# Optimization experiments

Measured on AMD Instinct MI355X. Metric: run time of the kernel, lower is better.

## Reference

```python
import jax, jax.numpy as jnp
import numpy as np

TEMPERATURE = 0.07
NEG_INF = -9e15
EPS = 1e-12

def setup_inputs() -> dict:
    key = jax.random.key(0)
    k1, k2 = jax.random.split(key)
    N, D = 8192, 128
    features = jax.random.normal(k1, (N, D), dtype=jnp.float32)
    labels = jax.random.randint(k2, (N,), 0, 16, dtype=jnp.int64)
    return {"features": features, "labels": labels}

def reference(features, labels):
    N = features.shape[0]
    # L2 normalize rows (torch F.normalize: x / max(||x||, eps))
    norm = jnp.linalg.norm(features, axis=1, keepdims=True)
    f = features / jnp.maximum(norm, EPS)
    # [N, N] similarity
    sim = jnp.matmul(f, f.T) / TEMPERATURE
    eye = jnp.eye(N, dtype=bool)
    sim = jnp.where(eye, NEG_INF, sim)
    # positive-pair mask: same label, excluding self
    pos_mask = ((labels[:, None] == labels[None, :]) & ~eye).astype(sim.dtype)
    denom = jnp.exp(sim).sum(axis=1, keepdims=True)  # [N, 1]
    log_prob = sim - jnp.log(denom + EPS)
    loss = -(pos_mask * log_prob).sum(axis=1) / (pos_mask.sum(axis=1) + EPS)
    return loss.mean()
```

## Files before the change

### kernel.cpp

```cpp
#include <hip/hip_runtime.h>
#include <hip/hip_bf16.h>

#define EPS 1e-12f
#define SQRT_C_EXP 4.53981597f
#define M_LN2F 0.69314718056f

#define BM 256
#define BN 128
#define KD 128
#define NCHUNK 8
#define NPART 16
#define PSTRIDE 48

typedef __attribute__((ext_vector_type(4))) float f32x4;
typedef __attribute__((ext_vector_type(8))) short bf16x8;

__device__ __forceinline__ float bf2f(ushort u) {
    unsigned int x = ((unsigned int)u) << 16;
    return __uint_as_float(x);
}

__device__ __forceinline__ void gload16(const void* g, void* l) {
    __builtin_amdgcn_global_load_lds(
        (const __attribute__((address_space(1))) void*)g,
        (__attribute__((address_space(3))) void*)l, 16, 0, 0);
}

__device__ __forceinline__ const bf16x8* lds_frag(const ushort* base, int r, int slot) {
    int sw = slot ^ (r & 7);
    return reinterpret_cast<const bf16x8*>(
        reinterpret_cast<const char*>(base) + r * 256 + sw * 16);
}

__global__ void normalize_kernel(const float* __restrict__ feat,
                                 ushort* __restrict__ fb,
                                 float* __restrict__ sq,
                                 int N) {
    int r    = (blockIdx.x * blockDim.x + threadIdx.x) >> 6;
    int lane = threadIdx.x & 63;
    if (r >= N) return;
    const float2 v = *reinterpret_cast<const float2*>(feat + (size_t)r * KD + lane * 2);
    float s = v.x * v.x + v.y * v.y;
    #pragma unroll
    for (int off = 1; off < 64; off <<= 1) s += __shfl_xor(s, off);
    const float scale = SQRT_C_EXP / fmaxf(sqrtf(s), EPS);

    __hip_bfloat16 h0 = __float2bfloat16(v.x * scale);
    __hip_bfloat16 h1 = __float2bfloat16(v.y * scale);
    ushort u0 = *reinterpret_cast<ushort*>(&h0);
    ushort u1 = *reinterpret_cast<ushort*>(&h1);
    unsigned int pack = (unsigned int)u0 | ((unsigned int)u1 << 16);
    *reinterpret_cast<unsigned int*>(fb + (size_t)r * KD + lane * 2) = pack;

    float q0 = bf2f(u0), q1 = bf2f(u1);
    float q = q0 * q0 + q1 * q1;
    #pragma unroll
    for (int off = 1; off < 64; off <<= 1) q += __shfl_xor(q, off);
    if (lane == 0) sq[r] = q;
}

__global__ __launch_bounds__(512)
__attribute__((amdgpu_waves_per_eu(2, 2)))
void supcon_denom(
    const ushort* __restrict__ fb,
    const int* __restrict__ labels,
    float* __restrict__ part,
    int N) {

    __shared__ __align__(16) ushort As[BM * KD];
    __shared__ __align__(16) ushort Bs[2][BN * KD];

    const int tid  = threadIdx.x;
    const int lane = tid & 63;
    const int w    = tid >> 6;
    const int wr   = w >> 1;
    const int wc   = w & 1;
    const int r16  = lane & 15;
    const int g4   = lane >> 4;

    const int rowbase = blockIdx.y * BM;
    const int col0    = blockIdx.x * (BN * NCHUNK);

    {
        const ushort* gA = fb + (size_t)rowbase * KD;
        #pragma unroll
        for (int i = 0; i < 8; i++) {
            int d = i * 512 + tid;
            int s = d ^ ((d >> 4) & 7);
            gload16(gA + (size_t)s * 8, &As[d * 8]);
        }
        const ushort* gB = fb + (size_t)col0 * KD;
        #pragma unroll
        for (int i = 0; i < 4; i++) {
            int d = i * 512 + tid;
            int s = d ^ ((d >> 4) & 7);
            gload16(gB + (size_t)s * 8, &Bs[0][d * 8]);
        }
    }

    int rlab[4][4];
    #pragma unroll
    for (int m = 0; m < 4; m++)
        #pragma unroll
        for (int i = 0; i < 4; i++)
            rlab[m][i] = labels[rowbase + wr * 64 + m * 16 + g4 * 4 + i];

    __syncthreads();

    bf16x8 a[4][4];
    #pragma unroll
    for (int ks = 0; ks < 4; ks++) {
        const int slot = ks * 4 + g4;
        #pragma unroll
        for (int m = 0; m < 4; m++)
            a[ks][m] = *lds_frag(As, wr * 64 + m * 16 + r16, slot);
    }

    float pd[4][4], pp[4][4], pc[4][4];
    #pragma unroll
    for (int m = 0; m < 4; m++)
        #pragma unroll
        for (int i = 0; i < 4; i++) { pd[m][i] = 0.f; pp[m][i] = 0.f; pc[m][i] = 0.f; }

    int cur = 0;
    for (int c = 0; c < NCHUNK; c++) {
        if (c + 1 < NCHUNK) {
            const ushort* gB = fb + (size_t)(col0 + (c + 1) * BN) * KD;
            ushort* dstb = Bs[cur ^ 1];
            #pragma unroll
            for (int i = 0; i < 4; i++) {
                int d = i * 512 + tid;
                int s = d ^ ((d >> 4) & 7);
                gload16(gB + (size_t)s * 8, &dstb[d * 8]);
            }
        }

        const ushort* bbase = Bs[cur];
        const int colbase = col0 + c * BN + wc * 64;

        #pragma unroll 1
        for (int n = 0; n < 4; n++) {
            const int clab = labels[colbase + n * 16 + r16];

            f32x4 acc[4];
            #pragma unroll
            for (int m = 0; m < 4; m++) acc[m] = f32x4{0.f, 0.f, 0.f, 0.f};

            #pragma unroll
            for (int ks = 0; ks < 4; ks++) {
                const int slot = ks * 4 + g4;
                bf16x8 bv = *lds_frag(bbase, wc * 64 + n * 16 + r16, slot);
                #pragma unroll
                for (int m = 0; m < 4; m++)
                    acc[m] = __builtin_amdgcn_mfma_f32_16x16x32_bf16(a[ks][m], bv, acc[m], 0, 0, 0);
            }

            #pragma unroll
            for (int m = 0; m < 4; m++)
                #pragma unroll
                for (int i = 0; i < 4; i++) {
                    const float sim = acc[m][i];
                    pd[m][i] += __builtin_amdgcn_exp2f(sim);
                    const bool mt = (rlab[m][i] == clab);
                    pp[m][i] += mt ? sim : 0.f;
                    pc[m][i] += mt ? 1.f : 0.f;
                }
        }

        __syncthreads();
        cur ^= 1;
    }

    #pragma unroll
    for (int off = 1; off < 16; off <<= 1)
        #pragma unroll
        for (int m = 0; m < 4; m++)
            #pragma unroll
            for (int i = 0; i < 4; i++) {
                pd[m][i] += __shfl_xor(pd[m][i], off);
                pp[m][i] += __shfl_xor(pp[m][i], off);
                pc[m][i] += __shfl_xor(pc[m][i], off);
            }

    if (r16 == 0) {
        const int slot = blockIdx.x * 2 + wc;
        #pragma unroll
        for (int m = 0; m < 4; m++)
            #pragma unroll
            for (int i = 0; i < 4; i++) {
                int r = rowbase + wr * 64 + m * 16 + g4 * 4 + i;
                float* p = part + (size_t)r * PSTRIDE + slot;
                p[0]  = pd[m][i];
                p[16] = pp[m][i];
                p[32] = pc[m][i];
            }
    }
}

__global__ void rowloss_kernel(const float* __restrict__ part,
                               const float* __restrict__ sq,
                               float* __restrict__ rowloss,
                               int N) {
    int r    = (blockIdx.x * blockDim.x + threadIdx.x) >> 6;
    int lane = threadIdx.x & 63;
    if (r >= N) return;

    float v = (lane < PSTRIDE) ? part[(size_t)r * PSTRIDE + lane] : 0.f;
    #pragma unroll
    for (int off = 1; off < 16; off <<= 1) v += __shfl_xor(v, off);
    float dsum = __shfl(v, 0);
    float psum = __shfl(v, 16);
    float csum = __shfl(v, 32);

    if (lane == 0) {
        float sqr    = sq[r];
        float possum = (psum - sqr) * M_LN2F;
        float cnt    = csum - 1.0f;
        float dn     = dsum - __builtin_amdgcn_exp2f(sqr);
        rowloss[r]   = -(possum - cnt * logf(dn + EPS)) / (cnt + EPS);
    }
}

__global__ void reduce_kernel(const float* __restrict__ rowloss,
                              float* __restrict__ out, int N) {
    __shared__ float sdata[16];
    float s = 0.f;
    for (int r = threadIdx.x; r < N; r += blockDim.x) s += rowloss[r];
    #pragma unroll
    for (int off = 1; off < 64; off <<= 1) s += __shfl_xor(s, off);
    int wv = threadIdx.x >> 6;
    if ((threadIdx.x & 63) == 0) sdata[wv] = s;
    __syncthreads();
    if (threadIdx.x == 0) {
        float t = 0.f;
        int nw = (int)(blockDim.x >> 6);
        for (int i = 0; i < nw; i++) t += sdata[i];
        out[0] = t / (float)N;
    }
}

extern "C" void kernel_launch(void* const* d_in, const int* in_sizes, int n_in,
                              void* d_out, int out_size, void* d_ws, size_t ws_size,
                              hipStream_t stream) {
    const float* feat = (const float*)d_in[0];
    const int* labels = (const int*)d_in[1];
    const int N = in_sizes[1];

    char* ws = (char*)d_ws;
    size_t off = 0;
    ushort* fb     = (ushort*)(ws + off);  off += (size_t)N * KD * sizeof(ushort);
    float* sq      = (float*)(ws + off);   off += (size_t)N * sizeof(float);
    float* part    = (float*)(ws + off);   off += (size_t)N * PSTRIDE * sizeof(float);
    float* rowloss = (float*)(ws + off);

    normalize_kernel<<<(N + 3) / 4, 256, 0, stream>>>(feat, fb, sq, N);

    dim3 grid(N / (BN * NCHUNK), N / BM);
    supcon_denom<<<grid, 512, 0, stream>>>(fb, labels, part, N);

    rowloss_kernel<<<(N + 3) / 4, 256, 0, stream>>>(part, sq, rowloss, N);
    reduce_kernel<<<1, 1024, 0, stream>>>(rowloss, (float*)d_out, N);
}
```

Baseline: 48.43 us.

## Compute positive counts from a class histogram and process two column tiles per iteration

```diff
diff --git a/kernel.cpp b/kernel.cpp
--- a/kernel.cpp
+++ b/kernel.cpp
@@ -4,13 +4,13 @@
 #define EPS 1e-12f
 #define SQRT_C_EXP 4.53981597f
 #define M_LN2F 0.69314718056f
+#define NUM_CLASSES 16
 
 #define BM 256
 #define BN 128
 #define KD 128
 #define NCHUNK 8
-#define NPART 16
-#define PSTRIDE 48
+#define PSTRIDE 32
 
 typedef __attribute__((ext_vector_type(4))) float f32x4;
 typedef __attribute__((ext_vector_type(8))) short bf16x8;
@@ -33,30 +33,61 @@
 }
 
 __global__ void normalize_kernel(const float* __restrict__ feat,
+                                 const int* __restrict__ labels,
                                  ushort* __restrict__ fb,
                                  float* __restrict__ sq,
+                                 float* __restrict__ cnt16,
                                  int N) {
-    int r    = (blockIdx.x * blockDim.x + threadIdx.x) >> 6;
-    int lane = threadIdx.x & 63;
-    if (r >= N) return;
-    const float2 v = *reinterpret_cast<const float2*>(feat + (size_t)r * KD + lane * 2);
-    float s = v.x * v.x + v.y * v.y;
-    #pragma unroll
-    for (int off = 1; off < 64; off <<= 1) s += __shfl_xor(s, off);
-    const float scale = SQRT_C_EXP / fmaxf(sqrtf(s), EPS);
-
-    __hip_bfloat16 h0 = __float2bfloat16(v.x * scale);
-    __hip_bfloat16 h1 = __float2bfloat16(v.y * scale);
-    ushort u0 = *reinterpret_cast<ushort*>(&h0);
-    ushort u1 = *reinterpret_cast<ushort*>(&h1);
-    unsigned int pack = (unsigned int)u0 | ((unsigned int)u1 << 16);
-    *reinterpret_cast<unsigned int*>(fb + (size_t)r * KD + lane * 2) = pack;
-
-    float q0 = bf2f(u0), q1 = bf2f(u1);
-    float q = q0 * q0 + q1 * q1;
-    #pragma unroll
-    for (int off = 1; off < 64; off <<= 1) q += __shfl_xor(q, off);
-    if (lane == 0) sq[r] = q;
+    const int tid  = threadIdx.x;
+    const int lane = tid & 63;
+    const int w    = tid >> 6;
+    int r = (blockIdx.x * blockDim.x + tid) >> 6;
+    if (r < N) {
+        const float2 v = *reinterpret_cast<const float2*>(feat + (size_t)r * KD + lane * 2);
+        float s = v.x * v.x + v.y * v.y;
+        #pragma unroll
+        for (int off = 1; off < 64; off <<= 1) s += __shfl_xor(s, off);
+        const float scale = SQRT_C_EXP / fmaxf(sqrtf(s), EPS);
+
+        __hip_bfloat16 h0 = __float2bfloat16(v.x * scale);
+        __hip_bfloat16 h1 = __float2bfloat16(v.y * scale);
+        ushort u0 = *reinterpret_cast<ushort*>(&h0);
+        ushort u1 = *reinterpret_cast<ushort*>(&h1);
+        unsigned int pack = (unsigned int)u0 | ((unsigned int)u1 << 16);
+        *reinterpret_cast<unsigned int*>(fb + (size_t)r * KD + lane * 2) = pack;
+
+        float q0 = bf2f(u0), q1 = bf2f(u1);
+        float q = q0 * q0 + q1 * q1;
+        #pragma unroll
+        for (int off = 1; off < 64; off <<= 1) q += __shfl_xor(q, off);
+        if (lane == 0) sq[r] = q;
+    }
+
+    if (blockIdx.x == 0) {
+        int cl[NUM_CLASSES];
+        #pragma unroll
+        for (int c = 0; c < NUM_CLASSES; c++) cl[c] = 0;
+        for (int i = tid; i < N; i += 256) {
+            int lb = labels[i];
+            #pragma unroll
+            for (int c = 0; c < NUM_CLASSES; c++) cl[c] += (lb == c) ? 1 : 0;
+        }
+        #pragma unroll
+        for (int c = 0; c < NUM_CLASSES; c++) {
+            int v = cl[c];
+            #pragma unroll
+            for (int off = 1; off < 64; off <<= 1) v += __shfl_xor(v, off);
+            cl[c] = v;
+        }
+        __shared__ int hw[4][NUM_CLASSES];
+        if (lane == 0) {
+            #pragma unroll
+            for (int c = 0; c < NUM_CLASSES; c++) hw[w][c] = cl[c];
+        }
+        __syncthreads();
+        if (tid < NUM_CLASSES)
+            cnt16[tid] = (float)(hw[0][tid] + hw[1][tid] + hw[2][tid] + hw[3][tid]);
+    }
 }
 
 __global__ __launch_bounds__(512)
@@ -116,11 +147,11 @@
             a[ks][m] = *lds_frag(As, wr * 64 + m * 16 + r16, slot);
     }
 
-    float pd[4][4], pp[4][4], pc[4][4];
+    float pd[4][4], pp[4][4];
     #pragma unroll
     for (int m = 0; m < 4; m++)
         #pragma unroll
-        for (int i = 0; i < 4; i++) { pd[m][i] = 0.f; pp[m][i] = 0.f; pc[m][i] = 0.f; }
+        for (int i = 0; i < 4; i++) { pd[m][i] = 0.f; pp[m][i] = 0.f; }
 
     int cur = 0;
     for (int c = 0; c < NCHUNK; c++) {
@@ -139,32 +170,42 @@
         const int colbase = col0 + c * BN + wc * 64;
 
         #pragma unroll 1
-        for (int n = 0; n < 4; n++) {
-            const int clab = labels[colbase + n * 16 + r16];
-
-            f32x4 acc[4];
-            #pragma unroll
-            for (int m = 0; m < 4; m++) acc[m] = f32x4{0.f, 0.f, 0.f, 0.f};
+        for (int n2 = 0; n2 < 2; n2++) {
+            int clab[2];
+            #pragma unroll
+            for (int j = 0; j < 2; j++)
+                clab[j] = labels[colbase + (n2 * 2 + j) * 16 + r16];
+
+            f32x4 acc[4][2];
+            #pragma unroll
+            for (int m = 0; m < 4; m++)
+                #pragma unroll
+                for (int j = 0; j < 2; j++) acc[m][j] = f32x4{0.f, 0.f, 0.f, 0.f};
 
             #pragma unroll
             for (int ks = 0; ks < 4; ks++) {
                 const int slot = ks * 4 + g4;
-                bf16x8 bv = *lds_frag(bbase, wc * 64 + n * 16 + r16, slot);
+                bf16x8 bv[2];
+                #pragma unroll
+                for (int j = 0; j < 2; j++)
+                    bv[j] = *lds_frag(bbase, wc * 64 + (n2 * 2 + j) * 16 + r16, slot);
                 #pragma unroll
                 for (int m = 0; m < 4; m++)
-                    acc[m] = __builtin_amdgcn_mfma_f32_16x16x32_bf16(a[ks][m], bv, acc[m], 0, 0, 0);
+                    #pragma unroll
+                    for (int j = 0; j < 2; j++)
+                        acc[m][j] = __builtin_amdgcn_mfma_f32_16x16x32_bf16(a[ks][m], bv[j], acc[m][j], 0, 0, 0);
             }
 
             #pragma unroll
             for (int m = 0; m < 4; m++)
                 #pragma unroll
-                for (int i = 0; i < 4; i++) {
-                    const float sim = acc[m][i];
-                    pd[m][i] += __builtin_amdgcn_exp2f(sim);
-                    const bool mt = (rlab[m][i] == clab);
-                    pp[m][i] += mt ? sim : 0.f;
-                    pc[m][i] += mt ? 1.f : 0.f;
-                }
+                for (int j = 0; j < 2; j++)
+                    #pragma unroll
+                    for (int i = 0; i < 4; i++) {
+                        const float sim = acc[m][j][i];
+                        pd[m][i] += __builtin_amdgcn_exp2f(sim);
+                        pp[m][i] += (rlab[m][i] == clab[j]) ? sim : 0.f;
+                    }
         }
 
         __syncthreads();
@@ -179,7 +220,6 @@
             for (int i = 0; i < 4; i++) {
                 pd[m][i] += __shfl_xor(pd[m][i], off);
                 pp[m][i] += __shfl_xor(pp[m][i], off);
-                pc[m][i] += __shfl_xor(pc[m][i], off);
             }
 
     if (r16 == 0) {
@@ -192,13 +232,14 @@
                 float* p = part + (size_t)r * PSTRIDE + slot;
                 p[0]  = pd[m][i];
                 p[16] = pp[m][i];
-                p[32] = pc[m][i];
             }
     }
 }
 
 __global__ void rowloss_kernel(const float* __restrict__ part,
                                const float* __restrict__ sq,
+                               const int* __restrict__ labels,
+                               const float* __restrict__ cnt16,
                                float* __restrict__ rowloss,
                                int N) {
     int r    = (blockIdx.x * blockDim.x + threadIdx.x) >> 6;
@@ -210,12 +251,11 @@
     for (int off = 1; off < 16; off <<= 1) v += __shfl_xor(v, off);
     float dsum = __shfl(v, 0);
     float psum = __shfl(v, 16);
-    float csum = __shfl(v, 32);
 
     if (lane == 0) {
         float sqr    = sq[r];
         float possum = (psum - sqr) * M_LN2F;
-        float cnt    = csum - 1.0f;
+        float cnt    = cnt16[labels[r]] - 1.0f;
         float dn     = dsum - __builtin_amdgcn_exp2f(sqr);
         rowloss[r]   = -(possum - cnt * logf(dn + EPS)) / (cnt + EPS);
     }
@@ -250,14 +290,15 @@
     size_t off = 0;
     ushort* fb     = (ushort*)(ws + off);  off += (size_t)N * KD * sizeof(ushort);
     float* sq      = (float*)(ws + off);   off += (size_t)N * sizeof(float);
+    float* cnt16   = (float*)(ws + off);   off += (size_t)NUM_CLASSES * sizeof(float);
     float* part    = (float*)(ws + off);   off += (size_t)N * PSTRIDE * sizeof(float);
     float* rowloss = (float*)(ws + off);
 
-    normalize_kernel<<<(N + 3) / 4, 256, 0, stream>>>(feat, fb, sq, N);
+    normalize_kernel<<<(N + 3) / 4, 256, 0, stream>>>(feat, labels, fb, sq, cnt16, N);
 
     dim3 grid(N / (BN * NCHUNK), N / BM);
     supcon_denom<<<grid, 512, 0, stream>>>(fb, labels, part, N);
 
-    rowloss_kernel<<<(N + 3) / 4, 256, 0, stream>>>(part, sq, rowloss, N);
+    rowloss_kernel<<<(N + 3) / 4, 256, 0, stream>>>(part, sq, labels, cnt16, rowloss, N);
     reduce_kernel<<<1, 1024, 0, stream>>>(rowloss, (float*)d_out, N);
 }
```

Result: slower. 50.31 us (+3.9%).
